# Optimization experiments

Hardware: AMD Instinct MI355X
Metric: run time of the kernel (lower is better)

The kernel has to match this reference:

```python
import jax, jax.numpy as jnp
import numpy as np

B, S, H = 2, 1024, 768
D, HID = 24, 96            # hdim_proj_dim, hdim_mlp_hidden
OUT_HID = 2 * max(128, H // 2)  # val_mlp hidden = 768
VAL_IN = 3 * H             # concat_hadam


def setup_inputs() -> dict:
    key = jax.random.key(0)
    ks = jax.random.split(key, 12)
    def w(k, shape, scale=0.02):
        return jax.random.normal(k, shape, dtype=jnp.float32) * scale
    return {
        "H_j": jax.random.normal(ks[0], (B, S, H), dtype=jnp.float32),
        "H_i": jax.random.normal(ks[1], (B, S, H), dtype=jnp.float32),
        "attn_mask": jnp.ones((B, S), dtype=jnp.float32),
        # p_j / p_i: Linear(H, D, bias=False), torch weight layout [D, H]
        "W_pj": w(ks[2], (D, H)),
        "W_pi": w(ks[3], (D, H)),
        # score_mlp: Linear(4D, HID) -> ReLU -> Linear(HID, 1)
        "W_s1": w(ks[4], (HID, 4 * D)),
        "b_s1": jnp.zeros((HID,), dtype=jnp.float32),
        "W_s2": w(ks[5], (1, HID)),
        "b_s2": jnp.zeros((1,), dtype=jnp.float32),
        # val_mlp: Linear(3H, OUT_HID) -> ReLU -> Linear(OUT_HID, H)
        "W_v1": w(ks[6], (OUT_HID, VAL_IN)),
        "b_v1": jnp.zeros((OUT_HID,), dtype=jnp.float32),
        "W_v2": w(ks[7], (H, OUT_HID)),
        "b_v2": jnp.zeros((H,), dtype=jnp.float32),
        "alpha": jnp.float32(0.05),  # init_gate_hdim
    }


def reference(H_j, H_i, attn_mask, W_pj, W_pi, W_s1, b_s1, W_s2, b_s2,
              W_v1, b_v1, W_v2, b_v2, alpha):
    # low-dim projections: [B,S,D]
    Zj = jnp.einsum('bsh,dh->bsd', H_j, W_pj)
    Zi = jnp.einsum('bsh,dh->bsd', H_i, W_pi)
    b, s, d = Zj.shape
    Zj_p = jnp.broadcast_to(Zj[:, :, None, :], (b, s, s, d))  # row = j (query)
    Zi_p = jnp.broadcast_to(Zi[:, None, :, :], (b, s, s, d))  # col = i (key)
    # 4-term pair features: [B,S,S,4D]
    pair = jnp.concatenate([Zj_p, Zi_p, Zj_p * Zi_p, jnp.abs(Zj_p - Zi_p)], axis=-1)
    # per-pair MLP -> scalar logit
    h = jax.nn.relu(jnp.einsum('bjif,hf->bjih', pair, W_s1) + b_s1)
    logits = jnp.einsum('bjih,oh->bjio', h, W_s2)[..., 0] + b_s2[0]  # [B,S,S]
    # additive key mask (mask over last dim = H_i positions)
    neg = jnp.finfo(logits.dtype).min
    logits = logits + (1.0 - attn_mask[:, None, :]) * neg
    # token_temp == 1.0 -> no temperature scaling
    probs = jax.nn.softmax(logits, axis=-1)
    ctx = jnp.einsum('bji,bih->bjh', probs, H_i)  # [B,S,H]
    # concat_hadam value features
    msg_in = jnp.concatenate([ctx, H_j, ctx * H_j], axis=-1)  # [B,S,3H]
    msg = jax.nn.relu(jnp.einsum('bsf,of->bso', msg_in, W_v1) + b_v1)
    msg = jnp.einsum('bso,ho->bsh', msg, W_v2) + b_v2
    # dropout is identity at inference; hdim_val_residual=False
    return alpha * msg
```

## Files before the change

kernel.cpp:

```cpp
#include <hip/hip_runtime.h>
#include <hip/hip_bf16.h>
#include <math.h>

#define B_ 2
#define S_ 1024
#define H_ 768
#define D_ 24
#define HID_ 96
#define OH_ 768
#define VI_ 2304

typedef short bf16x8 __attribute__((ext_vector_type(8)));
typedef _Float16 f16x8 __attribute__((ext_vector_type(8)));
typedef float f32x4 __attribute__((ext_vector_type(4)));
typedef unsigned short u16;

static __device__ __forceinline__ float relu_(float x) { return x > 0.f ? x : 0.f; }

static __device__ __forceinline__ short f2bf(float f) {
    __hip_bfloat16 h = __float2bfloat16(f);
    return *reinterpret_cast<short*>(&h);
}
static __device__ __forceinline__ float bf2f(short s) {
    unsigned u = ((unsigned)(u16)s) << 16;
    return __uint_as_float(u);
}

static __device__ __forceinline__ void gl_lds16(const void* g, void* l) {
    __builtin_amdgcn_global_load_lds(
        (const __attribute__((address_space(1))) unsigned int*)g,
        (__attribute__((address_space(3))) unsigned int*)l, 16, 0, 0);
}

#define NEGF (-3.402823466e38f)

__global__ __launch_bounds__(256) void proj_kernel(
    const float* __restrict__ Hj, const float* __restrict__ Hi,
    const float* __restrict__ Wpj, const float* __restrict__ Wpi,
    float* __restrict__ Zj, float* __restrict__ Zi)
{
    __shared__ float rowj[H_], rowi[H_];
    const int t = blockIdx.x;
    const int tid = threadIdx.x;
    const float* hj = Hj + (size_t)t * H_;
    const float* hi = Hi + (size_t)t * H_;
    for (int x = tid; x < H_; x += 256) { rowj[x] = hj[x]; rowi[x] = hi[x]; }
    __syncthreads();

    const int g = tid & 7;
    for (int o = tid >> 3; o < 2 * D_; o += 32) {
        const float* row;
        const float* w;
        if (o < D_) { row = rowj; w = Wpj + o * H_; }
        else        { row = rowi; w = Wpi + (o - D_) * H_; }
        float s = 0.f;
        #pragma unroll 8
        for (int c = 0; c < H_ / 8; ++c) s += row[g + 8 * c] * w[g + 8 * c];
        s += __shfl_down(s, 4, 8);
        s += __shfl_down(s, 2, 8);
        s += __shfl_down(s, 1, 8);
        if (g == 0) {
            if (o < D_) Zj[(size_t)t * D_ + o] = s;
            else        Zi[(size_t)t * D_ + (o - D_)] = s;
        }
    }
}

__global__ __launch_bounds__(256) void pair_mfma_kernel(
    const float* __restrict__ Zj, const float* __restrict__ Zi,
    const float* __restrict__ Ws1, const float* __restrict__ Ws2,
    const float* __restrict__ bs1, const float* __restrict__ bs2,
    float* __restrict__ P)
{
    __shared__ float    sZj32[16 * 32];
    __shared__ _Float16 sZj16[16 * 32];
    __shared__ _Float16 sZi16[128 * 64];
    __shared__ float    sAterm[16 * 96];
    __shared__ float    sW1a[96 * 25];
    __shared__ float    sW2[96];
    __shared__ float    sRed[4][64][4];

    const int j0 = blockIdx.x * 16, i0 = blockIdx.y * 128, b = blockIdx.z;
    const int tid = threadIdx.x;
    const int lane = tid & 63;
    const int wv = tid >> 6;
    const int q = lane & 15, g = lane >> 4;

    if (tid < 128) {
        int r = tid >> 3, d = tid & 7;
        float4 v = make_float4(0.f, 0.f, 0.f, 0.f);
        if (d < 6) v = *(const float4*)&Zj[((size_t)(b * S_ + j0 + r)) * D_ + 4 * d];
        *(float4*)&sZj32[r * 32 + 4 * d] = v;
        _Float16 h4[4] = {(_Float16)v.x, (_Float16)v.y, (_Float16)v.z, (_Float16)v.w};
        *(ushort4*)&sZj16[r * 32 + 4 * d] = *(const ushort4*)h4;
    }
    for (int t = tid; t < 512; t += 256) {
        int r = t >> 2, c = t & 3;
        int gr = c ^ (r & 7);
        f16x8 o = {0, 0, 0, 0, 0, 0, 0, 0};
        if (c < 3) {
            const float* src = &Zi[((size_t)(b * S_ + i0 + r)) * D_ + 8 * c];
            #pragma unroll
            for (int e = 0; e < 8; ++e) o[e] = (_Float16)src[e];
        }
        *(f16x8*)&sZi16[r * 64 + 8 * gr] = o;
    }
    for (int t = tid; t < 96 * 24; t += 256) {
        int k = t / 24, d = t - k * 24;
        sW1a[k * 25 + d] = Ws1[(size_t)k * 96 + d];
    }
    if (tid < 96) sW2[tid] = Ws2[tid];
    __syncthreads();

    for (int o = tid; o < 16 * 96; o += 256) {
        int j = o / 96, k = o - j * 96;
        float acc = bs1[k];
        #pragma unroll
        for (int d = 0; d < 24; ++d) acc += sW1a[k * 25 + d] * sZj32[j * 32 + d];
        sAterm[o] = acc;
    }

    f16x8 wf[3][6];
    #pragma unroll
    for (int s = 0; s < 3; ++s)
        #pragma unroll
        for (int nt = 0; nt < 6; ++nt) {
            f16x8 t8 = {0, 0, 0, 0, 0, 0, 0, 0};
            if (g < 3) {
                const float* wp = Ws1 + (size_t)(nt * 16 + q) * 96 + 24 * (s + 1) + 8 * g;
                #pragma unroll
                for (int e = 0; e < 8; ++e) t8[e] = (_Float16)wp[e];
            }
            wf[s][nt] = t8;
        }
    const float b2 = bs2[0];
    __syncthreads();

    f32x4 w2r[6];
    #pragma unroll
    for (int nt = 0; nt < 6; ++nt)
        w2r[nt] = *(const f32x4*)&sW2[nt * 16 + 4 * g];
    const f32x4 zero4 = {0.f, 0.f, 0.f, 0.f};

    for (int jq = 0; jq < 4; ++jq) {
        const int jj = wv * 4 + jq;
        const f16x8 zjh = *(const f16x8*)&sZj16[jj * 32 + 8 * g];
        f32x4 At[6];
        #pragma unroll
        for (int nt = 0; nt < 6; ++nt)
            At[nt] = *(const f32x4*)&sAterm[jj * 96 + nt * 16 + 4 * g];
        float* Prow = &P[((size_t)(b * S_ + j0 + jj)) * S_ + i0];

        for (int ibh = 0; ibh < 2; ++ibh) {
            #pragma unroll
            for (int ib4 = 0; ib4 < 4; ++ib4) {
                const int ii = (ibh * 4 + ib4) * 16 + q;
                const int sw = ii & 7;
                const f16x8 af1 = *(const f16x8*)&sZi16[ii * 64 + 8 * (g ^ sw)];
                const f16x8 a2 = zjh * af1;
                const f16x8 dd = zjh - af1;
                const f16x8 a3 = __builtin_elementwise_max(dd, -dd);

                f32x4 acc[6];
                #pragma unroll
                for (int nt = 0; nt < 6; ++nt) acc[nt] = At[nt];
                __builtin_amdgcn_s_setprio(1);
                #pragma unroll
                for (int nt = 0; nt < 6; ++nt) {
                    acc[nt] = __builtin_amdgcn_mfma_f32_16x16x32_f16(wf[0][nt], af1, acc[nt], 0, 0, 0);
                    acc[nt] = __builtin_amdgcn_mfma_f32_16x16x32_f16(wf[1][nt], a2,  acc[nt], 0, 0, 0);
                    acc[nt] = __builtin_amdgcn_mfma_f32_16x16x32_f16(wf[2][nt], a3,  acc[nt], 0, 0, 0);
                }
                __builtin_amdgcn_s_setprio(0);

                f32x4 lgv = zero4;
                #pragma unroll
                for (int nt = 0; nt < 6; ++nt)
                    lgv += w2r[nt] * __builtin_elementwise_max(acc[nt], zero4);
                sRed[wv][ib4 * 16 + q][g] = (lgv[0] + lgv[1]) + (lgv[2] + lgv[3]);
            }
            float4 v = *(const float4*)&sRed[wv][lane][0];
            Prow[ibh * 64 + lane] = (v.x + v.y) + (v.z + v.w) + b2;
        }
    }
}

__global__ __launch_bounds__(256) void softmax_kernel(
    const float* __restrict__ mask, const float* __restrict__ P,
    u16* __restrict__ Pb)
{
    const int r = blockIdx.x;
    const int b = r / S_;
    const int tid = threadIdx.x;
    const float* row = P + (size_t)r * S_;
    __shared__ float red[4];

    float v[4];
    float mx = -INFINITY;
    #pragma unroll
    for (int c = 0; c < 4; ++c) {
        int i = tid + 256 * c;
        float m = mask[b * S_ + i];
        v[c] = row[i] + (1.0f - m) * NEGF;
        mx = fmaxf(mx, v[c]);
    }
    for (int off = 32; off > 0; off >>= 1) mx = fmaxf(mx, __shfl_xor(mx, off));
    if ((tid & 63) == 0) red[tid >> 6] = mx;
    __syncthreads();
    mx = fmaxf(fmaxf(red[0], red[1]), fmaxf(red[2], red[3]));

    float s = 0.f;
    #pragma unroll
    for (int c = 0; c < 4; ++c) { v[c] = __expf(v[c] - mx); s += v[c]; }
    for (int off = 32; off > 0; off >>= 1) s += __shfl_xor(s, off);
    __syncthreads();
    if ((tid & 63) == 0) red[tid >> 6] = s;
    __syncthreads();
    s = red[0] + red[1] + red[2] + red[3];
    const float inv = 1.0f / s;
    #pragma unroll
    for (int c = 0; c < 4; ++c)
        Pb[(size_t)r * S_ + tid + 256 * c] = (u16)f2bf(v[c] * inv);
}

__global__ __launch_bounds__(256) void cvt_kernel(
    const float* __restrict__ src, u16* __restrict__ dst, int n4)
{
    int i = blockIdx.x * 256 + threadIdx.x;
    if (i >= n4) return;
    float4 v = ((const float4*)src)[i];
    ushort4 o;
    o.x = (u16)f2bf(v.x); o.y = (u16)f2bf(v.y);
    o.z = (u16)f2bf(v.z); o.w = (u16)f2bf(v.w);
    ((ushort4*)dst)[i] = o;
}

__global__ __launch_bounds__(256) void transpose_hi_kernel(
    const float* __restrict__ Hi, u16* __restrict__ HiT)
{
    __shared__ u16 t[32][33];
    const int i0 = blockIdx.x * 32, h0 = blockIdx.y * 32, b = blockIdx.z;
    const int c = threadIdx.x & 31, r = threadIdx.x >> 5;
    #pragma unroll
    for (int rr = r; rr < 32; rr += 8)
        t[rr][c] = (u16)f2bf(Hi[((size_t)(b * S_ + i0 + rr)) * H_ + h0 + c]);
    __syncthreads();
    #pragma unroll
    for (int rr = r; rr < 32; rr += 8)
        HiT[((size_t)(b * H_ + h0 + rr)) * S_ + i0 + c] = t[c][rr];
}

__global__ __launch_bounds__(256) void msgin_kernel(
    const u16* __restrict__ ctx, const float* __restrict__ Hj,
    u16* __restrict__ MSG)
{
    const int idx = blockIdx.x * 256 + threadIdx.x;
    const int m = idx / 96, c8 = (idx % 96) * 8;
    bf16x8 c = *(const bf16x8*)&ctx[(size_t)m * H_ + c8];
    float4 h0 = *(const float4*)&Hj[(size_t)m * H_ + c8];
    float4 h1 = *(const float4*)&Hj[(size_t)m * H_ + c8 + 4];
    float hf[8] = {h0.x, h0.y, h0.z, h0.w, h1.x, h1.y, h1.z, h1.w};
    bf16x8 hb, pb;
    #pragma unroll
    for (int e = 0; e < 8; ++e) {
        hb[e] = f2bf(hf[e]);
        pb[e] = f2bf(bf2f(c[e]) * hf[e]);
    }
    u16* row = MSG + (size_t)m * VI_;
    *(bf16x8*)&row[c8]        = c;
    *(bf16x8*)&row[768 + c8]  = hb;
    *(bf16x8*)&row[1536 + c8] = pb;
}

template<int MODE, int K>
__global__ __launch_bounds__(256) void mfma_gemm_kernel(
    const u16* __restrict__ Ag, const u16* __restrict__ Bg,
    const float* __restrict__ bias, const float* __restrict__ alphaPtr,
    void* __restrict__ Outv)
{
    __shared__ u16 As[2][64 * 64];
    __shared__ u16 Bs[2][64 * 64];
    const int tid = threadIdx.x;
    const int lane = tid & 63, wv = tid >> 6;
    const int q = lane & 15, g = lane >> 4;
    const int wr = wv >> 1, wc = wv & 1;
    const int m0 = blockIdx.x * 64, n0 = blockIdx.y * 64;

    const u16* Ab = Ag + (size_t)m0 * K;
    const u16* Bb = (MODE == 0)
        ? Bg + (size_t)(m0 >> 10) * H_ * S_ + (size_t)n0 * K
        : Bg + (size_t)n0 * K;

    int st_r[2], st_gc[2], st_dst[2];
    #pragma unroll
    for (int it = 0; it < 2; ++it) {
        int cidx = (it * 4 + wv) * 64 + lane;
        st_r[it] = cidx >> 3;
        st_gc[it] = (cidx & 7) ^ (st_r[it] & 7);
        st_dst[it] = cidx * 8;
    }

    f32x4 acc[2][2] = {};

    auto stage = [&](int buf, int k0) {
        #pragma unroll
        for (int it = 0; it < 2; ++it) {
            gl_lds16(Ab + (size_t)st_r[it] * K + k0 + st_gc[it] * 8,
                     &As[buf][st_dst[it]]);
            gl_lds16(Bb + (size_t)st_r[it] * K + k0 + st_gc[it] * 8,
                     &Bs[buf][st_dst[it]]);
        }
    };
    auto comp = [&](int buf) {
        #pragma unroll
        for (int ks = 0; ks < 2; ++ks) {
            bf16x8 af[2], bfr[2];
            #pragma unroll
            for (int m = 0; m < 2; ++m) {
                int r = wr * 32 + m * 16 + q;
                int cl = (g + ks * 4) ^ (r & 7);
                af[m] = *(const bf16x8*)&As[buf][r * 64 + cl * 8];
            }
            #pragma unroll
            for (int n = 0; n < 2; ++n) {
                int r = wc * 32 + n * 16 + q;
                int cl = (g + ks * 4) ^ (r & 7);
                bfr[n] = *(const bf16x8*)&Bs[buf][r * 64 + cl * 8];
            }
            #pragma unroll
            for (int m = 0; m < 2; ++m)
                #pragma unroll
                for (int n = 0; n < 2; ++n)
                    acc[m][n] = __builtin_amdgcn_mfma_f32_16x16x32_bf16(
                        af[m], bfr[n], acc[m][n], 0, 0, 0);
        }
    };

    constexpr int NT = K / 64;
    stage(0, 0);
    __syncthreads();
    int cur = 0;
    for (int kt = 0; kt < NT - 1; ++kt) {
        stage(cur ^ 1, (kt + 1) * 64);
        comp(cur);
        __syncthreads();
        cur ^= 1;
    }
    comp(cur);

    const float alpha = (MODE == 2) ? alphaPtr[0] : 0.f;
    u16* O16 = (u16*)Outv;
    float* Of = (float*)Outv;
    #pragma unroll
    for (int m = 0; m < 2; ++m) {
        #pragma unroll
        for (int n = 0; n < 2; ++n) {
            const int col = n0 + wc * 32 + n * 16 + q;
            const float bn = (MODE == 0) ? 0.f : bias[col];
            #pragma unroll
            for (int rg = 0; rg < 4; ++rg) {
                const int row = m0 + wr * 32 + m * 16 + g * 4 + rg;
                float v = acc[m][n][rg];
                if (MODE == 0)      O16[(size_t)row * H_ + col] = (u16)f2bf(v);
                else if (MODE == 1) O16[(size_t)row * H_ + col] = (u16)f2bf(relu_(v + bn));
                else                Of[(size_t)row * H_ + col] = alpha * (v + bn);
            }
        }
    }
}

extern "C" void kernel_launch(void* const* d_in, const int* in_sizes, int n_in,
                              void* d_out, int out_size, void* d_ws, size_t ws_size,
                              hipStream_t stream)
{
    (void)in_sizes; (void)n_in; (void)out_size; (void)ws_size;
    const float* Hj   = (const float*)d_in[0];
    const float* Hi   = (const float*)d_in[1];
    const float* mask = (const float*)d_in[2];
    const float* Wpj  = (const float*)d_in[3];
    const float* Wpi  = (const float*)d_in[4];
    const float* Ws1  = (const float*)d_in[5];
    const float* bs1  = (const float*)d_in[6];
    const float* Ws2  = (const float*)d_in[7];
    const float* bs2  = (const float*)d_in[8];
    const float* Wv1  = (const float*)d_in[9];
    const float* bv1  = (const float*)d_in[10];
    const float* Wv2  = (const float*)d_in[11];
    const float* bv2  = (const float*)d_in[12];
    const float* alphaPtr = (const float*)d_in[13];
    float* out = (float*)d_out;

    char* w = (char*)d_ws;
    float* Zj   = (float*)(w);
    float* Zi   = (float*)(w + 196608);
    size_t oPlog = 393216;
    size_t oPb   = oPlog + 8388608;
    size_t oHiT  = oPb + 4194304;
    size_t oWv1b = oHiT + 3145728;
    size_t oWv2b = oWv1b + 3538944;
    size_t oCTX  = oWv2b + 1179648;
    float* Plog = (float*)(w + oPlog);
    u16* Pb   = (u16*)(w + oPb);
    u16* HiT  = (u16*)(w + oHiT);
    u16* Wv1b = (u16*)(w + oWv1b);
    u16* Wv2b = (u16*)(w + oWv2b);
    u16* CTX  = (u16*)(w + oCTX);
    u16* MSG  = (u16*)(w + oPlog);
    u16* X1   = (u16*)(w + oHiT);

    cvt_kernel<<<(H_ * VI_ / 4 + 255) / 256, 256, 0, stream>>>(Wv1, Wv1b, H_ * VI_ / 4);
    cvt_kernel<<<(H_ * OH_ / 4 + 255) / 256, 256, 0, stream>>>(Wv2, Wv2b, H_ * OH_ / 4);
    transpose_hi_kernel<<<dim3(S_ / 32, H_ / 32, B_), 256, 0, stream>>>(Hi, HiT);

    proj_kernel<<<B_ * S_, 256, 0, stream>>>(Hj, Hi, Wpj, Wpi, Zj, Zi);
    pair_mfma_kernel<<<dim3(S_ / 16, S_ / 128, B_), 256, 0, stream>>>(
        Zj, Zi, Ws1, Ws2, bs1, bs2, Plog);
    softmax_kernel<<<B_ * S_, 256, 0, stream>>>(mask, Plog, Pb);

    mfma_gemm_kernel<0, S_><<<dim3(2048 / 64, H_ / 64), 256, 0, stream>>>(
        Pb, HiT, nullptr, nullptr, CTX);
    msgin_kernel<<<(2048 * 96) / 256, 256, 0, stream>>>(CTX, Hj, MSG);
    mfma_gemm_kernel<1, VI_><<<dim3(2048 / 64, OH_ / 64), 256, 0, stream>>>(
        MSG, Wv1b, bv1, nullptr, X1);
    mfma_gemm_kernel<2, OH_><<<dim3(2048 / 64, H_ / 64), 256, 0, stream>>>(
        X1, Wv2b, bv2, alphaPtr, out);
}
```

Baseline: 232.2 us.

## Fuse msg-input construction into ctx GEMM epilogue and batch projection tokens

Removes the separate msgin kernel. The first GEMM's epilogue now writes ctx, bf16(H_j) and ctx*H_j into three planar buffers, and the second GEMM reads its A operand plane by plane. The Ws1 fp16 MFMA fragments are precomputed once by a small kernel rather than converted per block in pair_mfma. The projection kernel now handles 4 tokens per block, reusing each weight load across the 4 tokens. The trade-offs are one extra launch and more epilogue stores in the ctx GEMM. The ctx*H_j product now uses fp32 ctx instead of bf16-rounded ctx.

```diff
diff --git a/kernel.cpp b/kernel.cpp
--- a/kernel.cpp
+++ b/kernel.cpp
@@ -9,6 +9,7 @@
 #define HID_ 96
 #define OH_ 768
 #define VI_ 2304
+#define PLANE_E 1572864
 
 typedef short bf16x8 __attribute__((ext_vector_type(8)));
 typedef _Float16 f16x8 __attribute__((ext_vector_type(8)));
@@ -21,10 +22,6 @@
     __hip_bfloat16 h = __float2bfloat16(f);
     return *reinterpret_cast<short*>(&h);
 }
-static __device__ __forceinline__ float bf2f(short s) {
-    unsigned u = ((unsigned)(u16)s) << 16;
-    return __uint_as_float(u);
-}
 
 static __device__ __forceinline__ void gl_lds16(const void* g, void* l) {
     __builtin_amdgcn_global_load_lds(
@@ -34,41 +31,78 @@
 
 #define NEGF (-3.402823466e38f)
 
+__global__ __launch_bounds__(256) void ws1frag_kernel(
+    const float* __restrict__ Ws1, u16* __restrict__ wfb)
+{
+    int idx = blockIdx.x * 256 + threadIdx.x;
+    if (idx >= 18 * 64) return;
+    int frag = idx >> 6, lane = idx & 63;
+    int s = frag / 6, nt = frag - s * 6, q = lane & 15, g = lane >> 4;
+    u16 out[8] = {0, 0, 0, 0, 0, 0, 0, 0};
+    if (g < 3) {
+        const float* wp = Ws1 + (size_t)(nt * 16 + q) * 96 + 24 * (s + 1) + 8 * g;
+        #pragma unroll
+        for (int e = 0; e < 8; ++e) {
+            _Float16 h = (_Float16)wp[e];
+            out[e] = *reinterpret_cast<u16*>(&h);
+        }
+    }
+    *(ushort4*)&wfb[idx * 8]     = make_ushort4(out[0], out[1], out[2], out[3]);
+    *(ushort4*)&wfb[idx * 8 + 4] = make_ushort4(out[4], out[5], out[6], out[7]);
+}
+
 __global__ __launch_bounds__(256) void proj_kernel(
     const float* __restrict__ Hj, const float* __restrict__ Hi,
     const float* __restrict__ Wpj, const float* __restrict__ Wpi,
     float* __restrict__ Zj, float* __restrict__ Zi)
 {
-    __shared__ float rowj[H_], rowi[H_];
-    const int t = blockIdx.x;
+    __shared__ float rTj[H_ * 4], rTi[H_ * 4];
+    const int t0 = blockIdx.x * 4;
     const int tid = threadIdx.x;
-    const float* hj = Hj + (size_t)t * H_;
-    const float* hi = Hi + (size_t)t * H_;
-    for (int x = tid; x < H_; x += 256) { rowj[x] = hj[x]; rowi[x] = hi[x]; }
+    for (int x = tid; x < 4 * H_; x += 256) {
+        int tok = x / H_, cc = x - tok * H_;
+        rTj[cc * 4 + tok] = Hj[(size_t)(t0 + tok) * H_ + cc];
+        rTi[cc * 4 + tok] = Hi[(size_t)(t0 + tok) * H_ + cc];
+    }
     __syncthreads();
 
     const int g = tid & 7;
-    for (int o = tid >> 3; o < 2 * D_; o += 32) {
-        const float* row;
-        const float* w;
-        if (o < D_) { row = rowj; w = Wpj + o * H_; }
-        else        { row = rowi; w = Wpi + (o - D_) * H_; }
-        float s = 0.f;
+    #pragma unroll
+    for (int oo = 0; oo < 2; ++oo) {
+        const int o = (tid >> 3) + oo * 32;
+        if (o >= 48) break;
+        const bool isJ = o < 24;
+        const float* w = isJ ? (Wpj + (size_t)o * H_) : (Wpi + (size_t)(o - 24) * H_);
+        const float* rT = isJ ? rTj : rTi;
+        float s0 = 0.f, s1 = 0.f, s2 = 0.f, s3 = 0.f;
         #pragma unroll 8
-        for (int c = 0; c < H_ / 8; ++c) s += row[g + 8 * c] * w[g + 8 * c];
-        s += __shfl_down(s, 4, 8);
-        s += __shfl_down(s, 2, 8);
-        s += __shfl_down(s, 1, 8);
+        for (int c = 0; c < H_ / 8; ++c) {
+            float wv = w[g + 8 * c];
+            float4 rv = *(const float4*)&rT[(g + 8 * c) * 4];
+            s0 += rv.x * wv; s1 += rv.y * wv; s2 += rv.z * wv; s3 += rv.w * wv;
+        }
+        #pragma unroll
+        for (int off = 4; off > 0; off >>= 1) {
+            s0 += __shfl_down(s0, off, 8);
+            s1 += __shfl_down(s1, off, 8);
+            s2 += __shfl_down(s2, off, 8);
+            s3 += __shfl_down(s3, off, 8);
+        }
         if (g == 0) {
-            if (o < D_) Zj[(size_t)t * D_ + o] = s;
-            else        Zi[(size_t)t * D_ + (o - D_)] = s;
+            float* dst = isJ ? Zj : Zi;
+            const int oc = isJ ? o : (o - 24);
+            dst[(size_t)(t0 + 0) * D_ + oc] = s0;
+            dst[(size_t)(t0 + 1) * D_ + oc] = s1;
+            dst[(size_t)(t0 + 2) * D_ + oc] = s2;
+            dst[(size_t)(t0 + 3) * D_ + oc] = s3;
         }
     }
 }
 
 __global__ __launch_bounds__(256) void pair_mfma_kernel(
     const float* __restrict__ Zj, const float* __restrict__ Zi,
-    const float* __restrict__ Ws1, const float* __restrict__ Ws2,
+    const float* __restrict__ Ws1, const u16* __restrict__ wfbuf,
+    const float* __restrict__ Ws2,
     const float* __restrict__ bs1, const float* __restrict__ bs2,
     float* __restrict__ P)
 {
@@ -110,6 +144,14 @@
         sW1a[k * 25 + d] = Ws1[(size_t)k * 96 + d];
     }
     if (tid < 96) sW2[tid] = Ws2[tid];
+
+    f16x8 wf[3][6];
+    #pragma unroll
+    for (int s = 0; s < 3; ++s)
+        #pragma unroll
+        for (int nt = 0; nt < 6; ++nt)
+            wf[s][nt] = *(const f16x8*)&wfbuf[((s * 6 + nt) * 64 + lane) * 8];
+    const float b2 = bs2[0];
     __syncthreads();
 
     for (int o = tid; o < 16 * 96; o += 256) {
@@ -119,21 +161,6 @@
         for (int d = 0; d < 24; ++d) acc += sW1a[k * 25 + d] * sZj32[j * 32 + d];
         sAterm[o] = acc;
     }
-
-    f16x8 wf[3][6];
-    #pragma unroll
-    for (int s = 0; s < 3; ++s)
-        #pragma unroll
-        for (int nt = 0; nt < 6; ++nt) {
-            f16x8 t8 = {0, 0, 0, 0, 0, 0, 0, 0};
-            if (g < 3) {
-                const float* wp = Ws1 + (size_t)(nt * 16 + q) * 96 + 24 * (s + 1) + 8 * g;
-                #pragma unroll
-                for (int e = 0; e < 8; ++e) t8[e] = (_Float16)wp[e];
-            }
-            wf[s][nt] = t8;
-        }
-    const float b2 = bs2[0];
     __syncthreads();
 
     f32x4 w2r[6];
@@ -250,28 +277,6 @@
         HiT[((size_t)(b * H_ + h0 + rr)) * S_ + i0 + c] = t[c][rr];
 }
 
-__global__ __launch_bounds__(256) void msgin_kernel(
-    const u16* __restrict__ ctx, const float* __restrict__ Hj,
-    u16* __restrict__ MSG)
-{
-    const int idx = blockIdx.x * 256 + threadIdx.x;
-    const int m = idx / 96, c8 = (idx % 96) * 8;
-    bf16x8 c = *(const bf16x8*)&ctx[(size_t)m * H_ + c8];
-    float4 h0 = *(const float4*)&Hj[(size_t)m * H_ + c8];
-    float4 h1 = *(const float4*)&Hj[(size_t)m * H_ + c8 + 4];
-    float hf[8] = {h0.x, h0.y, h0.z, h0.w, h1.x, h1.y, h1.z, h1.w};
-    bf16x8 hb, pb;
-    #pragma unroll
-    for (int e = 0; e < 8; ++e) {
-        hb[e] = f2bf(hf[e]);
-        pb[e] = f2bf(bf2f(c[e]) * hf[e]);
-    }
-    u16* row = MSG + (size_t)m * VI_;
-    *(bf16x8*)&row[c8]        = c;
-    *(bf16x8*)&row[768 + c8]  = hb;
-    *(bf16x8*)&row[1536 + c8] = pb;
-}
-
 template<int MODE, int K>
 __global__ __launch_bounds__(256) void mfma_gemm_kernel(
     const u16* __restrict__ Ag, const u16* __restrict__ Bg,
@@ -286,7 +291,6 @@
     const int wr = wv >> 1, wc = wv & 1;
     const int m0 = blockIdx.x * 64, n0 = blockIdx.y * 64;
 
-    const u16* Ab = Ag + (size_t)m0 * K;
     const u16* Bb = (MODE == 0)
         ? Bg + (size_t)(m0 >> 10) * H_ * S_ + (size_t)n0 * K
         : Bg + (size_t)n0 * K;
@@ -303,9 +307,20 @@
     f32x4 acc[2][2] = {};
 
     auto stage = [&](int buf, int k0) {
+        const u16* Asrc;
+        int kk;
+        if (MODE == 1) {
+            int pl = k0 / 768;
+            kk = k0 - pl * 768;
+            Asrc = Ag + (size_t)pl * PLANE_E + (size_t)m0 * 768;
+        } else {
+            Asrc = Ag + (size_t)m0 * K;
+            kk = k0;
+        }
+        const int AST = (MODE == 1) ? 768 : K;
         #pragma unroll
         for (int it = 0; it < 2; ++it) {
-            gl_lds16(Ab + (size_t)st_r[it] * K + k0 + st_gc[it] * 8,
+            gl_lds16(Asrc + (size_t)st_r[it] * AST + kk + st_gc[it] * 8,
                      &As[buf][st_dst[it]]);
             gl_lds16(Bb + (size_t)st_r[it] * K + k0 + st_gc[it] * 8,
                      &Bs[buf][st_dst[it]]);
@@ -361,9 +376,16 @@
             for (int rg = 0; rg < 4; ++rg) {
                 const int row = m0 + wr * 32 + m * 16 + g * 4 + rg;
                 float v = acc[m][n][rg];
-                if (MODE == 0)      O16[(size_t)row * H_ + col] = (u16)f2bf(v);
-                else if (MODE == 1) O16[(size_t)row * H_ + col] = (u16)f2bf(relu_(v + bn));
-                else                Of[(size_t)row * H_ + col] = alpha * (v + bn);
+                if (MODE == 0) {
+                    float hj = bias[(size_t)row * H_ + col];
+                    O16[(size_t)row * H_ + col]               = (u16)f2bf(v);
+                    O16[PLANE_E + (size_t)row * H_ + col]     = (u16)f2bf(hj);
+                    O16[2 * PLANE_E + (size_t)row * H_ + col] = (u16)f2bf(v * hj);
+                } else if (MODE == 1) {
+                    O16[(size_t)row * H_ + col] = (u16)f2bf(relu_(v + bn));
+                } else {
+                    Of[(size_t)row * H_ + col] = alpha * (v + bn);
+                }
             }
         }
     }
@@ -393,35 +415,29 @@
     char* w = (char*)d_ws;
     float* Zj   = (float*)(w);
     float* Zi   = (float*)(w + 196608);
-    size_t oPlog = 393216;
-    size_t oPb   = oPlog + 8388608;
-    size_t oHiT  = oPb + 4194304;
-    size_t oWv1b = oHiT + 3145728;
-    size_t oWv2b = oWv1b + 3538944;
-    size_t oCTX  = oWv2b + 1179648;
-    float* Plog = (float*)(w + oPlog);
-    u16* Pb   = (u16*)(w + oPb);
-    u16* HiT  = (u16*)(w + oHiT);
-    u16* Wv1b = (u16*)(w + oWv1b);
-    u16* Wv2b = (u16*)(w + oWv2b);
-    u16* CTX  = (u16*)(w + oCTX);
-    u16* MSG  = (u16*)(w + oPlog);
-    u16* X1   = (u16*)(w + oHiT);
-
+    float* Plog = (float*)(w + 393216);
+    u16* MSGp  = (u16*)(w + 393216);
+    u16* Pb    = (u16*)(w + 9830400);
+    u16* HiT   = (u16*)(w + 14024704);
+    u16* X1    = (u16*)(w + 14024704);
+    u16* Wv1b  = (u16*)(w + 17170432);
+    u16* Wv2b  = (u16*)(w + 20709376);
+    u16* wfbuf = (u16*)(w + 21889024);
+
+    ws1frag_kernel<<<5, 256, 0, stream>>>(Ws1, wfbuf);
     cvt_kernel<<<(H_ * VI_ / 4 + 255) / 256, 256, 0, stream>>>(Wv1, Wv1b, H_ * VI_ / 4);
     cvt_kernel<<<(H_ * OH_ / 4 + 255) / 256, 256, 0, stream>>>(Wv2, Wv2b, H_ * OH_ / 4);
     transpose_hi_kernel<<<dim3(S_ / 32, H_ / 32, B_), 256, 0, stream>>>(Hi, HiT);
 
-    proj_kernel<<<B_ * S_, 256, 0, stream>>>(Hj, Hi, Wpj, Wpi, Zj, Zi);
+    proj_kernel<<<B_ * S_ / 4, 256, 0, stream>>>(Hj, Hi, Wpj, Wpi, Zj, Zi);
     pair_mfma_kernel<<<dim3(S_ / 16, S_ / 128, B_), 256, 0, stream>>>(
-        Zj, Zi, Ws1, Ws2, bs1, bs2, Plog);
+        Zj, Zi, Ws1, wfbuf, Ws2, bs1, bs2, Plog);
     softmax_kernel<<<B_ * S_, 256, 0, stream>>>(mask, Plog, Pb);
 
     mfma_gemm_kernel<0, S_><<<dim3(2048 / 64, H_ / 64), 256, 0, stream>>>(
-        Pb, HiT, nullptr, nullptr, CTX);
-    msgin_kernel<<<(2048 * 96) / 256, 256, 0, stream>>>(CTX, Hj, MSG);
+        Pb, HiT, Hj, nullptr, MSGp);
     mfma_gemm_kernel<1, VI_><<<dim3(2048 / 64, OH_ / 64), 256, 0, stream>>>(
-        MSG, Wv1b, bv1, nullptr, X1);
+        MSGp, Wv1b, bv1, nullptr, X1);
     mfma_gemm_kernel<2, OH_><<<dim3(2048 / 64, H_ / 64), 256, 0, stream>>>(
         X1, Wv2b, bv2, alphaPtr, out);
 }
```

Measured after the change: 219.4 us. 1.06x faster.
